# Optimization experiments

Measured on AMD Instinct MI355X. Metric: run time of the kernel, lower is better.

Reference implementation:

```python
import jax, jax.numpy as jnp
import numpy as np

N = 50000   # nodes
E = 800000  # edges (before self loops)
D = 128     # feature dim (n_feat == all n_units due to fusion-cat constraint)
BN_EPS = 1e-5


def _gcn_norm(edge_index, edge_weight, n):
    # PyG gcn_norm with add_self_loops=True (self-loop weight 1.0)
    loop = jnp.arange(n)
    row = jnp.concatenate([edge_index[0], loop])
    col = jnp.concatenate([edge_index[1], loop])
    w = jnp.concatenate([edge_weight, jnp.ones((n,), edge_weight.dtype)])
    deg = jax.ops.segment_sum(w, col, num_segments=n)  # [N]
    deg_safe = jnp.where(deg > 0, deg, 1.0)
    dis = jnp.where(deg > 0, jax.lax.rsqrt(deg_safe), 0.0)
    norm = dis[row] * w * dis[col]  # [E+N]
    return row, col, norm


def _gcn_conv(x, row, col, norm, W, b):
    # out_i = sum_{j->i} norm_ij * (x_j @ W) + b
    h = x @ W                                   # [N, Dout]
    msg = norm[:, None] * h[row]                # gather + scale, [E+N, Dout]
    out = jax.ops.segment_sum(msg, col, num_segments=x.shape[0])
    return out + b


def setup_inputs() -> dict:
    key = jax.random.key(0)
    ks = jax.random.split(key, 9)
    emb = jax.random.normal(ks[0], (N, D), jnp.float32)
    edge_index = jax.random.randint(ks[1], (2, E), 0, N)
    edge_weight = jax.random.uniform(ks[2], (E,), jnp.float32)
    W0 = jax.random.normal(ks[3], (D, D), jnp.float32) / np.sqrt(D).astype(np.float32)
    b0 = jnp.zeros((D,), jnp.float32)
    W1 = jax.random.normal(ks[4], (D, D), jnp.float32) / np.sqrt(D).astype(np.float32)
    b1 = jnp.zeros((D,), jnp.float32)
    bn_gamma = jax.random.uniform(ks[5], (D,), jnp.float32, 0.5, 1.5)
    bn_beta = jax.random.normal(ks[6], (D,), jnp.float32) * 0.1
    bn_mean = jax.random.normal(ks[7], (D,), jnp.float32) * 0.1
    bn_var = jax.random.uniform(ks[8], (D,), jnp.float32, 0.5, 1.5)
    return dict(emb=emb, edge_index=edge_index, edge_weight=edge_weight,
                W0=W0, b0=b0, W1=W1, b1=b1,
                bn_gamma=bn_gamma, bn_beta=bn_beta, bn_mean=bn_mean, bn_var=bn_var)


def reference(emb, edge_index, edge_weight, W0, b0, W1, b1,
              bn_gamma, bn_beta, bn_mean, bn_var):
    n = emb.shape[0]
    row, col, norm = _gcn_norm(edge_index, edge_weight, n)
    # loop runs once (batchnorm_stack has len 1 -> zip truncates):
    h1 = _gcn_conv(emb, row, col, norm, W0, b0)
    h1 = (h1 - bn_mean) * jax.lax.rsqrt(bn_var + BN_EPS) * bn_gamma + bn_beta
    h1 = jax.nn.elu(h1)  # dropout is identity in eval mode
    # final layer applied outside loop, no BN/ELU:
    h2 = _gcn_conv(h1, row, col, norm, W1, b1)
    # fusion: mean over [emb, h1, h2] along the stacked scale axis
    return (emb + h1 + h2) / 3.0
```

## Files before the change

### kernel.cpp

```cpp
#include <hip/hip_runtime.h>
#include <hip/hip_fp16.h>
#include <math.h>

#define BN_EPS 1e-5f
#define CAP 48
#define ABLK 8192

typedef __attribute__((ext_vector_type(8))) short bf16x8;
typedef __attribute__((ext_vector_type(4))) float f32x4;

__device__ __forceinline__ unsigned short f2b(float f) {
    unsigned u = __float_as_uint(f);
    return (unsigned short)((u + 0x7fffu + ((u >> 16) & 1u)) >> 16);
}
__device__ __forceinline__ unsigned pack2(float lo, float hi) {
    return (unsigned)f2b(lo) | ((unsigned)f2b(hi) << 16);
}
__device__ __forceinline__ float slot_w(unsigned s) {
    return __half2float(__ushort_as_half((unsigned short)(s & 0xffffu)));
}
__device__ __forceinline__ float4 b2f4(ushort4 u) {
    return make_float4(__uint_as_float((unsigned)u.x << 16),
                       __uint_as_float((unsigned)u.y << 16),
                       __uint_as_float((unsigned)u.z << 16),
                       __uint_as_float((unsigned)u.w << 16));
}

__global__ __launch_bounds__(1024) void k_bin(
        const int* __restrict__ erow, const int* __restrict__ ecol,
        const float* __restrict__ ew,
        uint2* __restrict__ binned, unsigned short* __restrict__ Hs,
        int E, int NA, int nbins,
        const float* __restrict__ W0, const float* __restrict__ W1,
        const float* __restrict__ emb,
        unsigned short* __restrict__ wp0, unsigned short* __restrict__ wp1,
        unsigned short* __restrict__ embB, int n) {
    int bb = blockIdx.x;
    int t = threadIdx.x;
    if (bb < NA) {
        __shared__ unsigned sHist[256];
        __shared__ unsigned sStart[257];
        __shared__ unsigned sCur[256];
        if (t < 256) sHist[t] = 0;
        __syncthreads();
        int base = bb * ABLK;
        int m = E - base; if (m > ABLK) m = ABLK;
        int er[8]; int ec[8]; float ewt[8];
        int i0 = t * 8;
        if (i0 + 8 <= m) {
            int4 ra = *(const int4*)(erow + base + i0);
            int4 rb = *(const int4*)(erow + base + i0 + 4);
            int4 ca = *(const int4*)(ecol + base + i0);
            int4 cb = *(const int4*)(ecol + base + i0 + 4);
            float4 wa = *(const float4*)(ew + base + i0);
            float4 wb = *(const float4*)(ew + base + i0 + 4);
            er[0] = ra.x; er[1] = ra.y; er[2] = ra.z; er[3] = ra.w;
            er[4] = rb.x; er[5] = rb.y; er[6] = rb.z; er[7] = rb.w;
            ec[0] = ca.x; ec[1] = ca.y; ec[2] = ca.z; ec[3] = ca.w;
            ec[4] = cb.x; ec[5] = cb.y; ec[6] = cb.z; ec[7] = cb.w;
            ewt[0] = wa.x; ewt[1] = wa.y; ewt[2] = wa.z; ewt[3] = wa.w;
            ewt[4] = wb.x; ewt[5] = wb.y; ewt[6] = wb.z; ewt[7] = wb.w;
        } else {
            #pragma unroll
            for (int k = 0; k < 8; ++k) {
                int i = i0 + k;
                if (i < m) { er[k] = erow[base + i]; ec[k] = ecol[base + i]; ewt[k] = ew[base + i]; }
                else { er[k] = 0; ec[k] = -1; ewt[k] = 0.f; }
            }
        }
        #pragma unroll
        for (int k = 0; k < 8; ++k)
            if (ec[k] >= 0) atomicAdd(&sHist[ec[k] >> 8], 1u);
        __syncthreads();
        if (t < 64) {
            unsigned carry = 0;
            #pragma unroll
            for (int c = 0; c < 4; ++c) {
                unsigned v = sHist[c * 64 + t];
                unsigned inc = v;
                #pragma unroll
                for (int d = 1; d < 64; d <<= 1) {
                    unsigned y = __shfl_up(inc, d);
                    if (t >= d) inc += y;
                }
                unsigned ex = carry + inc - v;
                sStart[c * 64 + t] = ex;
                sCur[c * 64 + t] = ex;
                carry += __shfl(inc, 63);
            }
            if (t == 0) sStart[256] = carry;
        }
        __syncthreads();
        if (t <= nbins) Hs[(size_t)bb * 256 + t] = (unsigned short)sStart[t];
        #pragma unroll
        for (int k = 0; k < 8; ++k) {
            if (ec[k] >= 0) {
                int bn = ec[k] >> 8;
                unsigned pos = atomicAdd(&sCur[bn], 1u);
                binned[(size_t)base + pos] =
                    make_uint2(((unsigned)er[k] << 8) | ((unsigned)ec[k] & 255u),
                               __float_as_uint(ewt[k]));
            }
        }
    } else {
        int b2 = bb - NA;
        if (b2 < 4) {
            int tid = b2 * 1024 + t;
            const float* W = (tid < 2048) ? W0 : W1;
            unsigned short* wp = (tid < 2048) ? wp0 : wp1;
            int f = tid & 2047;
            int q = f >> 9;
            int tt = (f >> 6) & 7;
            int l = f & 63;
            int col = tt * 16 + (l & 15);
            int k0 = q * 32 + (l >> 4) * 8;
            unsigned short o[8];
            #pragma unroll
            for (int j = 0; j < 8; ++j) o[j] = f2b(W[(k0 + j) * 128 + col]);
            *(uint4*)(wp + (size_t)f * 8) = *(uint4*)o;
        } else {
            int idx = (b2 - 4) * 1024 + t;
            if (idx < n * 16) {
                const float4* src = (const float4*)emb + (size_t)idx * 2;
                float4 v0 = src[0], v1 = src[1];
                uint4 o;
                o.x = pack2(v0.x, v0.y); o.y = pack2(v0.z, v0.w);
                o.z = pack2(v1.x, v1.y); o.w = pack2(v1.z, v1.w);
                ((uint4*)embB)[idx] = o;
            }
        }
    }
}

__global__ __launch_bounds__(1024) void k_build(
        const uint2* __restrict__ binned, const unsigned short* __restrict__ Hs,
        int NA, unsigned* __restrict__ eEdge, int* __restrict__ cnt,
        float* __restrict__ dis, int n) {
    __shared__ unsigned cntL[256];
    __shared__ float wsumL[256];
    int t = threadIdx.x;
    if (t < 256) { cntL[t] = 0; wsumL[t] = 0.f; }
    __syncthreads();
    int b = blockIdx.x;
    int node0 = b << 8;
    int wv = t >> 6, lane = t & 63;
    for (int s = wv; s < NA; s += 16) {
        int start = Hs[(size_t)s * 256 + b];
        int end   = Hs[(size_t)s * 256 + b + 1];
        size_t sb = (size_t)s * ABLK;
        for (int o = start + lane; o < end; o += 64) {
            uint2 rec = binned[sb + o];
            unsigned d = rec.x & 255u;
            unsigned r = rec.x >> 8;
            float w = __uint_as_float(rec.y);
            unsigned p = atomicAdd(&cntL[d], 1u);
            if (p < CAP)
                eEdge[(size_t)(node0 + (int)d) * CAP + p] =
                    (r << 16) | (unsigned)__half_as_ushort(__float2half(w));
            atomicAdd(&wsumL[d], w);
        }
    }
    __syncthreads();
    if (t < 256) {
        int node = node0 + t;
        if (node < n) {
            unsigned c = cntL[t]; if (c > CAP) c = CAP;
            cnt[node] = (int)c;
            dis[node] = rsqrtf(wsumL[t] + 1.0f);
        }
    }
}

__device__ __forceinline__ void agg_node(const unsigned* __restrict__ ep,
                                         const unsigned short* __restrict__ h,
                                         const float* __restrict__ dis,
                                         float disc, int c, int lane,
                                         float acc[8]) {
    int g = lane >> 4;
    int fo = (lane & 15) * 8;
    for (int j = 0; j < c; j += 16) {
        unsigned s[4];
        int r[4];
        float d[4], nm[4];
        uint4 u[4];
        #pragma unroll
        for (int k = 0; k < 4; ++k) s[k] = ep[j + 4 * k + g];
        #pragma unroll
        for (int k = 0; k < 4; ++k) r[k] = (j + 4 * k + g < c) ? (int)(s[k] >> 16) : 0;
        #pragma unroll
        for (int k = 0; k < 4; ++k) d[k] = dis[r[k]];
        #pragma unroll
        for (int k = 0; k < 4; ++k) u[k] = *(const uint4*)(h + ((size_t)r[k] << 7) + fo);
        #pragma unroll
        for (int k = 0; k < 4; ++k)
            nm[k] = (j + 4 * k + g < c) ? d[k] * slot_w(s[k]) * disc : 0.f;
        #pragma unroll
        for (int k = 0; k < 4; ++k) {
            acc[0] += nm[k] * __uint_as_float(u[k].x << 16);
            acc[1] += nm[k] * __uint_as_float(u[k].x & 0xffff0000u);
            acc[2] += nm[k] * __uint_as_float(u[k].y << 16);
            acc[3] += nm[k] * __uint_as_float(u[k].y & 0xffff0000u);
            acc[4] += nm[k] * __uint_as_float(u[k].z << 16);
            acc[5] += nm[k] * __uint_as_float(u[k].z & 0xffff0000u);
            acc[6] += nm[k] * __uint_as_float(u[k].w << 16);
            acc[7] += nm[k] * __uint_as_float(u[k].w & 0xffff0000u);
        }
    }
    #pragma unroll
    for (int f = 0; f < 8; ++f) {
        acc[f] += __shfl_xor(acc[f], 16);
        acc[f] += __shfl_xor(acc[f], 32);
    }
}

__global__ __launch_bounds__(1024) void k_conv1(
        const int* __restrict__ cnt, const unsigned* __restrict__ eEdge,
        const unsigned short* __restrict__ embB, const float* __restrict__ dis,
        const unsigned short* __restrict__ wp,
        const float* __restrict__ b0, const float* __restrict__ gamma,
        const float* __restrict__ beta, const float* __restrict__ mean,
        const float* __restrict__ var,
        unsigned short* __restrict__ h1b, int n) {
    __shared__ unsigned short sWp[16384];
    __shared__ unsigned short sA[16 * 136];
    int t = threadIdx.x;
    { uint4* d = (uint4*)sWp; const uint4* s = (const uint4*)wp;
      d[t] = s[t]; d[t + 1024] = s[t + 1024]; }
    int w = t >> 6;
    int lane = t & 63;
    int wid = blockIdx.x * 16 + w;
    bool valid = wid < n;
    int c = valid ? __builtin_amdgcn_readfirstlane(cnt[wid]) : 0;
    float disc = valid ? dis[wid] : 0.f;
    float acc[8] = {};
    agg_node(eEdge + (size_t)wid * CAP, embB, dis, disc, c, lane, acc);
    if (lane < 16) {
        int fo = lane * 8;
        float s2 = disc * disc;
        uint4 hu = make_uint4(0, 0, 0, 0);
        if (valid) hu = *(const uint4*)(embB + ((size_t)wid << 7) + fo);
        acc[0] += s2 * __uint_as_float(hu.x << 16);
        acc[1] += s2 * __uint_as_float(hu.x & 0xffff0000u);
        acc[2] += s2 * __uint_as_float(hu.y << 16);
        acc[3] += s2 * __uint_as_float(hu.y & 0xffff0000u);
        acc[4] += s2 * __uint_as_float(hu.z << 16);
        acc[5] += s2 * __uint_as_float(hu.z & 0xffff0000u);
        acc[6] += s2 * __uint_as_float(hu.w << 16);
        acc[7] += s2 * __uint_as_float(hu.w & 0xffff0000u);
        uint4 o;
        o.x = pack2(acc[0], acc[1]); o.y = pack2(acc[2], acc[3]);
        o.z = pack2(acc[4], acc[5]); o.w = pack2(acc[6], acc[7]);
        *(uint4*)(sA + w * 136 + fo) = o;
    }
    __syncthreads();
    int m = lane & 15, quad = lane >> 4;
    f32x4 c2 = {0.f, 0.f, 0.f, 0.f};
    if (w < 8) {
        #pragma unroll
        for (int q = 0; q < 4; ++q) {
            bf16x8 a = *(const bf16x8*)(sA + m * 136 + q * 32 + quad * 8);
            bf16x8 b = *(const bf16x8*)(sWp + (size_t)((q * 8 + w) * 64 + lane) * 8);
            c2 = __builtin_amdgcn_mfma_f32_16x16x32_bf16(a, b, c2, 0, 0, 0);
        }
    }
    __syncthreads();
    if (w < 8) {
        int col = w * 16 + m;
        float bias = b0[col];
        float mn = mean[col], bt = beta[col];
        float iv = rsqrtf(var[col] + BN_EPS) * gamma[col];
        #pragma unroll
        for (int r = 0; r < 4; ++r) {
            float x = c2[r] + bias;
            x = (x - mn) * iv + bt;
            x = x > 0.f ? x : expm1f(x);
            sA[(quad * 4 + r) * 136 + col] = f2b(x);
        }
    }
    __syncthreads();
    if (t < 256) {
        int r = t >> 4, c8 = (t & 15) * 8;
        int node = blockIdx.x * 16 + r;
        if (node < n)
            *(uint4*)(h1b + ((size_t)node << 7) + c8) = *(const uint4*)(sA + r * 136 + c8);
    }
}

__global__ __launch_bounds__(1024) void k_conv2(
        const int* __restrict__ cnt, const unsigned* __restrict__ eEdge,
        const unsigned short* __restrict__ h1b, const float* __restrict__ dis,
        const unsigned short* __restrict__ wp,
        const float* __restrict__ b1, const float* __restrict__ emb,
        float* __restrict__ out, int n) {
    __shared__ unsigned short sWp[16384];
    __shared__ unsigned short sA[16 * 136];
    __shared__ float sC[16 * 132];
    int t = threadIdx.x;
    { uint4* d = (uint4*)sWp; const uint4* s = (const uint4*)wp;
      d[t] = s[t]; d[t + 1024] = s[t + 1024]; }
    int w = t >> 6;
    int lane = t & 63;
    int wid = blockIdx.x * 16 + w;
    bool valid = wid < n;
    int c = valid ? __builtin_amdgcn_readfirstlane(cnt[wid]) : 0;
    float disc = valid ? dis[wid] : 0.f;
    float acc[8] = {};
    agg_node(eEdge + (size_t)wid * CAP, h1b, dis, disc, c, lane, acc);
    if (lane < 16) {
        int fo = lane * 8;
        float s2 = disc * disc;
        uint4 hu = make_uint4(0, 0, 0, 0);
        if (valid) hu = *(const uint4*)(h1b + ((size_t)wid << 7) + fo);
        acc[0] += s2 * __uint_as_float(hu.x << 16);
        acc[1] += s2 * __uint_as_float(hu.x & 0xffff0000u);
        acc[2] += s2 * __uint_as_float(hu.y << 16);
        acc[3] += s2 * __uint_as_float(hu.y & 0xffff0000u);
        acc[4] += s2 * __uint_as_float(hu.z << 16);
        acc[5] += s2 * __uint_as_float(hu.z & 0xffff0000u);
        acc[6] += s2 * __uint_as_float(hu.w << 16);
        acc[7] += s2 * __uint_as_float(hu.w & 0xffff0000u);
        uint4 o;
        o.x = pack2(acc[0], acc[1]); o.y = pack2(acc[2], acc[3]);
        o.z = pack2(acc[4], acc[5]); o.w = pack2(acc[6], acc[7]);
        *(uint4*)(sA + w * 136 + fo) = o;
    }
    __syncthreads();
    int m = lane & 15, quad = lane >> 4;
    f32x4 c2 = {0.f, 0.f, 0.f, 0.f};
    if (w < 8) {
        #pragma unroll
        for (int q = 0; q < 4; ++q) {
            bf16x8 a = *(const bf16x8*)(sA + m * 136 + q * 32 + quad * 8);
            bf16x8 b = *(const bf16x8*)(sWp + (size_t)((q * 8 + w) * 64 + lane) * 8);
            c2 = __builtin_amdgcn_mfma_f32_16x16x32_bf16(a, b, c2, 0, 0, 0);
        }
        int col = w * 16 + m;
        float bias = b1[col];
        #pragma unroll
        for (int r = 0; r < 4; ++r)
            sC[(quad * 4 + r) * 132 + col] = c2[r] + bias;
    }
    __syncthreads();
    if (t < 512) {
        int r = t >> 5, c4 = (t & 31) * 4;
        int node = blockIdx.x * 16 + r;
        if (node < n) {
            float4 cc = *(const float4*)(sC + r * 132 + c4);
            float4 ev = *(const float4*)(emb + ((size_t)node << 7) + c4);
            float4 hv = b2f4(*(const ushort4*)(h1b + ((size_t)node << 7) + c4));
            const float third = 1.0f / 3.0f;
            float4 o;
            o.x = (ev.x + hv.x + cc.x) * third;
            o.y = (ev.y + hv.y + cc.y) * third;
            o.z = (ev.z + hv.z + cc.z) * third;
            o.w = (ev.w + hv.w + cc.w) * third;
            *(float4*)(out + ((size_t)node << 7) + c4) = o;
        }
    }
}

extern "C" void kernel_launch(void* const* d_in, const int* in_sizes, int n_in,
                              void* d_out, int out_size, void* d_ws, size_t ws_size,
                              hipStream_t stream) {
    const float* emb   = (const float*)d_in[0];
    const int*   eidx  = (const int*)d_in[1];
    const float* ew    = (const float*)d_in[2];
    const float* W0    = (const float*)d_in[3];
    const float* b0    = (const float*)d_in[4];
    const float* W1    = (const float*)d_in[5];
    const float* b1    = (const float*)d_in[6];
    const float* gamma = (const float*)d_in[7];
    const float* beta  = (const float*)d_in[8];
    const float* mean  = (const float*)d_in[9];
    const float* var   = (const float*)d_in[10];

    const int n = in_sizes[0] / 128;
    const int E = in_sizes[2];
    const int* rowp = eidx;
    const int* colp = eidx + E;

    char* ws = (char*)d_ws;
    unsigned short* embB = (unsigned short*)ws;
    unsigned short* h1b  = (unsigned short*)(ws + (size_t)n * 256);
    uint2* binned = (uint2*)h1b;
    char* p = ws + (size_t)n * 512;
    float* dis  = (float*)p;
    int*   cnt  = (int*)  (p + (size_t)n * 4);
    unsigned short* wp0 = (unsigned short*)(p + (size_t)n * 8);
    unsigned short* wp1 = (unsigned short*)(p + (size_t)n * 8 + 32768);
    unsigned short* Hs  = (unsigned short*)(p + (size_t)n * 8 + 65536);
    unsigned* eEdge = (unsigned*)(p + (size_t)n * 8 + 131072);
    float* outf = (float*)d_out;

    const int NA    = (E + ABLK - 1) / ABLK;
    const int PB    = 4 + (n * 16 + 1023) / 1024;
    const int nbins = (n + 255) >> 8;
    const int cb    = (n + 15) / 16;

    k_bin<<<NA + PB, 1024, 0, stream>>>(rowp, colp, ew, binned, Hs, E, NA, nbins,
                                        W0, W1, emb, wp0, wp1, embB, n);
    k_build<<<nbins, 1024, 0, stream>>>(binned, Hs, NA, eEdge, cnt, dis, n);
    k_conv1<<<cb, 1024, 0, stream>>>(cnt, eEdge, embB, dis, wp0,
                                     b0, gamma, beta, mean, var, h1b, n);
    k_conv2<<<cb, 1024, 0, stream>>>(cnt, eEdge, h1b, dis, wp1,
                                     b1, emb, outf, n);
}
```

Measured before the change: 199.7 us.

## Fuse all stages into one cooperative persistent kernel with grid syncs

Merges binning, CSR build, and both GCN conv layers into a single persistent kernel launched cooperatively, separated by grid-wide syncs, with a phased multi-launch fallback. It aims to remove inter-kernel launch gaps and tail effects. Binned edge records are also staged in shared memory and written to global memory in a coalesced pass instead of scattered writes. The cost is grid-sync overhead, a grid limited by occupancy of large-shared-memory 1024-thread blocks, and fewer concurrent blocks for the build phase.

Result: slower. 652.4 us (+226.6%).

```diff
diff --git a/kernel.cpp b/kernel.cpp
--- a/kernel.cpp
+++ b/kernel.cpp
@@ -1,6 +1,9 @@
 #include <hip/hip_runtime.h>
+#include <hip/hip_cooperative_groups.h>
 #include <hip/hip_fp16.h>
 #include <math.h>
+
+namespace cg = cooperative_groups;
 
 #define BN_EPS 1e-5f
 #define CAP 48
@@ -24,151 +27,6 @@
                        __uint_as_float((unsigned)u.y << 16),
                        __uint_as_float((unsigned)u.z << 16),
                        __uint_as_float((unsigned)u.w << 16));
-}
-
-__global__ __launch_bounds__(1024) void k_bin(
-        const int* __restrict__ erow, const int* __restrict__ ecol,
-        const float* __restrict__ ew,
-        uint2* __restrict__ binned, unsigned short* __restrict__ Hs,
-        int E, int NA, int nbins,
-        const float* __restrict__ W0, const float* __restrict__ W1,
-        const float* __restrict__ emb,
-        unsigned short* __restrict__ wp0, unsigned short* __restrict__ wp1,
-        unsigned short* __restrict__ embB, int n) {
-    int bb = blockIdx.x;
-    int t = threadIdx.x;
-    if (bb < NA) {
-        __shared__ unsigned sHist[256];
-        __shared__ unsigned sStart[257];
-        __shared__ unsigned sCur[256];
-        if (t < 256) sHist[t] = 0;
-        __syncthreads();
-        int base = bb * ABLK;
-        int m = E - base; if (m > ABLK) m = ABLK;
-        int er[8]; int ec[8]; float ewt[8];
-        int i0 = t * 8;
-        if (i0 + 8 <= m) {
-            int4 ra = *(const int4*)(erow + base + i0);
-            int4 rb = *(const int4*)(erow + base + i0 + 4);
-            int4 ca = *(const int4*)(ecol + base + i0);
-            int4 cb = *(const int4*)(ecol + base + i0 + 4);
-            float4 wa = *(const float4*)(ew + base + i0);
-            float4 wb = *(const float4*)(ew + base + i0 + 4);
-            er[0] = ra.x; er[1] = ra.y; er[2] = ra.z; er[3] = ra.w;
-            er[4] = rb.x; er[5] = rb.y; er[6] = rb.z; er[7] = rb.w;
-            ec[0] = ca.x; ec[1] = ca.y; ec[2] = ca.z; ec[3] = ca.w;
-            ec[4] = cb.x; ec[5] = cb.y; ec[6] = cb.z; ec[7] = cb.w;
-            ewt[0] = wa.x; ewt[1] = wa.y; ewt[2] = wa.z; ewt[3] = wa.w;
-            ewt[4] = wb.x; ewt[5] = wb.y; ewt[6] = wb.z; ewt[7] = wb.w;
-        } else {
-            #pragma unroll
-            for (int k = 0; k < 8; ++k) {
-                int i = i0 + k;
-                if (i < m) { er[k] = erow[base + i]; ec[k] = ecol[base + i]; ewt[k] = ew[base + i]; }
-                else { er[k] = 0; ec[k] = -1; ewt[k] = 0.f; }
-            }
-        }
-        #pragma unroll
-        for (int k = 0; k < 8; ++k)
-            if (ec[k] >= 0) atomicAdd(&sHist[ec[k] >> 8], 1u);
-        __syncthreads();
-        if (t < 64) {
-            unsigned carry = 0;
-            #pragma unroll
-            for (int c = 0; c < 4; ++c) {
-                unsigned v = sHist[c * 64 + t];
-                unsigned inc = v;
-                #pragma unroll
-                for (int d = 1; d < 64; d <<= 1) {
-                    unsigned y = __shfl_up(inc, d);
-                    if (t >= d) inc += y;
-                }
-                unsigned ex = carry + inc - v;
-                sStart[c * 64 + t] = ex;
-                sCur[c * 64 + t] = ex;
-                carry += __shfl(inc, 63);
-            }
-            if (t == 0) sStart[256] = carry;
-        }
-        __syncthreads();
-        if (t <= nbins) Hs[(size_t)bb * 256 + t] = (unsigned short)sStart[t];
-        #pragma unroll
-        for (int k = 0; k < 8; ++k) {
-            if (ec[k] >= 0) {
-                int bn = ec[k] >> 8;
-                unsigned pos = atomicAdd(&sCur[bn], 1u);
-                binned[(size_t)base + pos] =
-                    make_uint2(((unsigned)er[k] << 8) | ((unsigned)ec[k] & 255u),
-                               __float_as_uint(ewt[k]));
-            }
-        }
-    } else {
-        int b2 = bb - NA;
-        if (b2 < 4) {
-            int tid = b2 * 1024 + t;
-            const float* W = (tid < 2048) ? W0 : W1;
-            unsigned short* wp = (tid < 2048) ? wp0 : wp1;
-            int f = tid & 2047;
-            int q = f >> 9;
-            int tt = (f >> 6) & 7;
-            int l = f & 63;
-            int col = tt * 16 + (l & 15);
-            int k0 = q * 32 + (l >> 4) * 8;
-            unsigned short o[8];
-            #pragma unroll
-            for (int j = 0; j < 8; ++j) o[j] = f2b(W[(k0 + j) * 128 + col]);
-            *(uint4*)(wp + (size_t)f * 8) = *(uint4*)o;
-        } else {
-            int idx = (b2 - 4) * 1024 + t;
-            if (idx < n * 16) {
-                const float4* src = (const float4*)emb + (size_t)idx * 2;
-                float4 v0 = src[0], v1 = src[1];
-                uint4 o;
-                o.x = pack2(v0.x, v0.y); o.y = pack2(v0.z, v0.w);
-                o.z = pack2(v1.x, v1.y); o.w = pack2(v1.z, v1.w);
-                ((uint4*)embB)[idx] = o;
-            }
-        }
-    }
-}
-
-__global__ __launch_bounds__(1024) void k_build(
-        const uint2* __restrict__ binned, const unsigned short* __restrict__ Hs,
-        int NA, unsigned* __restrict__ eEdge, int* __restrict__ cnt,
-        float* __restrict__ dis, int n) {
-    __shared__ unsigned cntL[256];
-    __shared__ float wsumL[256];
-    int t = threadIdx.x;
-    if (t < 256) { cntL[t] = 0; wsumL[t] = 0.f; }
-    __syncthreads();
-    int b = blockIdx.x;
-    int node0 = b << 8;
-    int wv = t >> 6, lane = t & 63;
-    for (int s = wv; s < NA; s += 16) {
-        int start = Hs[(size_t)s * 256 + b];
-        int end   = Hs[(size_t)s * 256 + b + 1];
-        size_t sb = (size_t)s * ABLK;
-        for (int o = start + lane; o < end; o += 64) {
-            uint2 rec = binned[sb + o];
-            unsigned d = rec.x & 255u;
-            unsigned r = rec.x >> 8;
-            float w = __uint_as_float(rec.y);
-            unsigned p = atomicAdd(&cntL[d], 1u);
-            if (p < CAP)
-                eEdge[(size_t)(node0 + (int)d) * CAP + p] =
-                    (r << 16) | (unsigned)__half_as_ushort(__float2half(w));
-            atomicAdd(&wsumL[d], w);
-        }
-    }
-    __syncthreads();
-    if (t < 256) {
-        int node = node0 + t;
-        if (node < n) {
-            unsigned c = cntL[t]; if (c > CAP) c = CAP;
-            cnt[node] = (int)c;
-            dis[node] = rsqrtf(wsumL[t] + 1.0f);
-        }
-    }
 }
 
 __device__ __forceinline__ void agg_node(const unsigned* __restrict__ ep,
@@ -213,148 +71,301 @@
     }
 }
 
-__global__ __launch_bounds__(1024) void k_conv1(
-        const int* __restrict__ cnt, const unsigned* __restrict__ eEdge,
-        const unsigned short* __restrict__ embB, const float* __restrict__ dis,
-        const unsigned short* __restrict__ wp,
-        const float* __restrict__ b0, const float* __restrict__ gamma,
-        const float* __restrict__ beta, const float* __restrict__ mean,
-        const float* __restrict__ var,
-        unsigned short* __restrict__ h1b, int n) {
-    __shared__ unsigned short sWp[16384];
-    __shared__ unsigned short sA[16 * 136];
+__global__ __launch_bounds__(1024, 8) void k_mega(
+        const int* __restrict__ erow, const int* __restrict__ ecol,
+        const float* __restrict__ ew,
+        uint2* __restrict__ binned, unsigned short* __restrict__ Hs,
+        unsigned* __restrict__ eEdge, int* __restrict__ cnt, float* __restrict__ dis,
+        const float* __restrict__ W0, const float* __restrict__ W1,
+        const float* __restrict__ emb,
+        unsigned short* __restrict__ wp0, unsigned short* __restrict__ wp1,
+        unsigned short* __restrict__ embB,
+        const float* __restrict__ b0v, const float* __restrict__ gammav,
+        const float* __restrict__ betav, const float* __restrict__ meanv,
+        const float* __restrict__ varv, const float* __restrict__ b1v,
+        unsigned short* __restrict__ h1b, float* __restrict__ out,
+        int n, int E, int NA, int PB, int phase) {
+    __shared__ __align__(16) char smem[68624];
     int t = threadIdx.x;
-    { uint4* d = (uint4*)sWp; const uint4* s = (const uint4*)wp;
-      d[t] = s[t]; d[t + 1024] = s[t + 1024]; }
+    const int nblk = gridDim.x;
+    const int gb = (n + 255) >> 8;
+    const int cb = (n + 15) >> 4;
+
+    if (phase == 0 || phase == 1) {
+        unsigned* sHist  = (unsigned*)smem;
+        unsigned* sStart = sHist + 256;
+        unsigned* sCur   = sStart + 257;
+        uint2*    sRec   = (uint2*)(smem + 3080);
+        for (int item = blockIdx.x; item < NA + PB; item += nblk) {
+            __syncthreads();
+            if (item < NA) {
+                if (t < 256) sHist[t] = 0;
+                __syncthreads();
+                int base = item * ABLK;
+                int m = E - base; if (m > ABLK) m = ABLK;
+                int er[8]; int ec[8]; float ewt[8];
+                int i0 = t * 8;
+                if (i0 + 8 <= m) {
+                    int4 ra = *(const int4*)(erow + base + i0);
+                    int4 rb = *(const int4*)(erow + base + i0 + 4);
+                    int4 ca = *(const int4*)(ecol + base + i0);
+                    int4 cb4 = *(const int4*)(ecol + base + i0 + 4);
+                    float4 wa = *(const float4*)(ew + base + i0);
+                    float4 wb = *(const float4*)(ew + base + i0 + 4);
+                    er[0] = ra.x; er[1] = ra.y; er[2] = ra.z; er[3] = ra.w;
+                    er[4] = rb.x; er[5] = rb.y; er[6] = rb.z; er[7] = rb.w;
+                    ec[0] = ca.x; ec[1] = ca.y; ec[2] = ca.z; ec[3] = ca.w;
+                    ec[4] = cb4.x; ec[5] = cb4.y; ec[6] = cb4.z; ec[7] = cb4.w;
+                    ewt[0] = wa.x; ewt[1] = wa.y; ewt[2] = wa.z; ewt[3] = wa.w;
+                    ewt[4] = wb.x; ewt[5] = wb.y; ewt[6] = wb.z; ewt[7] = wb.w;
+                } else {
+                    #pragma unroll
+                    for (int k = 0; k < 8; ++k) {
+                        int i = i0 + k;
+                        if (i < m) { er[k] = erow[base + i]; ec[k] = ecol[base + i]; ewt[k] = ew[base + i]; }
+                        else { er[k] = 0; ec[k] = -1; ewt[k] = 0.f; }
+                    }
+                }
+                #pragma unroll
+                for (int k = 0; k < 8; ++k)
+                    if (ec[k] >= 0) atomicAdd(&sHist[ec[k] >> 8], 1u);
+                __syncthreads();
+                if (t < 64) {
+                    unsigned carry = 0;
+                    #pragma unroll
+                    for (int c4 = 0; c4 < 4; ++c4) {
+                        unsigned v = sHist[c4 * 64 + t];
+                        unsigned inc = v;
+                        #pragma unroll
+                        for (int d = 1; d < 64; d <<= 1) {
+                            unsigned y = __shfl_up(inc, d);
+                            if (t >= d) inc += y;
+                        }
+                        unsigned ex = carry + inc - v;
+                        sStart[c4 * 64 + t] = ex;
+                        sCur[c4 * 64 + t] = ex;
+                        carry += __shfl(inc, 63);
+                    }
+                    if (t == 0) sStart[256] = carry;
+                }
+                __syncthreads();
+                if (t <= gb) Hs[(size_t)item * 256 + t] = (unsigned short)sStart[t];
+                #pragma unroll
+                for (int k = 0; k < 8; ++k) {
+                    if (ec[k] >= 0) {
+                        int bn = ec[k] >> 8;
+                        unsigned pos = atomicAdd(&sCur[bn], 1u);
+                        sRec[pos] = make_uint2(((unsigned)er[k] << 8) | ((unsigned)ec[k] & 255u),
+                                               __float_as_uint(ewt[k]));
+                    }
+                }
+                __syncthreads();
+                for (int i = t; i < m; i += 1024) binned[(size_t)base + i] = sRec[i];
+            } else {
+                int b2 = item - NA;
+                if (b2 < 4) {
+                    int tid = b2 * 1024 + t;
+                    const float* W = (tid < 2048) ? W0 : W1;
+                    unsigned short* wp = (tid < 2048) ? wp0 : wp1;
+                    int f = tid & 2047;
+                    int q = f >> 9;
+                    int tt = (f >> 6) & 7;
+                    int l = f & 63;
+                    int col = tt * 16 + (l & 15);
+                    int k0 = q * 32 + (l >> 4) * 8;
+                    unsigned short o[8];
+                    #pragma unroll
+                    for (int j = 0; j < 8; ++j) o[j] = f2b(W[(k0 + j) * 128 + col]);
+                    *(uint4*)(wp + (size_t)f * 8) = *(uint4*)o;
+                } else {
+                    int idx = (b2 - 4) * 1024 + t;
+                    if (idx < n * 16) {
+                        const float4* src = (const float4*)emb + (size_t)idx * 2;
+                        float4 v0 = src[0], v1 = src[1];
+                        uint4 o;
+                        o.x = pack2(v0.x, v0.y); o.y = pack2(v0.z, v0.w);
+                        o.z = pack2(v1.x, v1.y); o.w = pack2(v1.z, v1.w);
+                        ((uint4*)embB)[idx] = o;
+                    }
+                }
+            }
+        }
+    }
+    if (phase == 0) { __threadfence(); cg::this_grid().sync(); }
+
+    if (phase == 0 || phase == 2) {
+        unsigned* cntL = (unsigned*)smem;
+        float* wsumL = (float*)(smem + 1024);
+        for (int b = blockIdx.x; b < gb; b += nblk) {
+            __syncthreads();
+            if (t < 256) { cntL[t] = 0; wsumL[t] = 0.f; }
+            __syncthreads();
+            int node0 = b << 8;
+            int wv = t >> 6, lane = t & 63;
+            for (int s = wv; s < NA; s += 16) {
+                int start = Hs[(size_t)s * 256 + b];
+                int end   = Hs[(size_t)s * 256 + b + 1];
+                size_t sb = (size_t)s * ABLK;
+                for (int o = start + lane; o < end; o += 64) {
+                    uint2 rec = binned[sb + o];
+                    unsigned d = rec.x & 255u;
+                    unsigned r = rec.x >> 8;
+                    float w = __uint_as_float(rec.y);
+                    unsigned p = atomicAdd(&cntL[d], 1u);
+                    if (p < CAP)
+                        eEdge[(size_t)(node0 + (int)d) * CAP + p] =
+                            (r << 16) | (unsigned)__half_as_ushort(__float2half(w));
+                    atomicAdd(&wsumL[d], w);
+                }
+            }
+            __syncthreads();
+            if (t < 256) {
+                int node = node0 + t;
+                if (node < n) {
+                    unsigned c = cntL[t]; if (c > CAP) c = CAP;
+                    cnt[node] = (int)c;
+                    dis[node] = rsqrtf(wsumL[t] + 1.0f);
+                }
+            }
+        }
+    }
+    if (phase == 0) { __threadfence(); cg::this_grid().sync(); }
+
     int w = t >> 6;
     int lane = t & 63;
-    int wid = blockIdx.x * 16 + w;
-    bool valid = wid < n;
-    int c = valid ? __builtin_amdgcn_readfirstlane(cnt[wid]) : 0;
-    float disc = valid ? dis[wid] : 0.f;
-    float acc[8] = {};
-    agg_node(eEdge + (size_t)wid * CAP, embB, dis, disc, c, lane, acc);
-    if (lane < 16) {
-        int fo = lane * 8;
-        float s2 = disc * disc;
-        uint4 hu = make_uint4(0, 0, 0, 0);
-        if (valid) hu = *(const uint4*)(embB + ((size_t)wid << 7) + fo);
-        acc[0] += s2 * __uint_as_float(hu.x << 16);
-        acc[1] += s2 * __uint_as_float(hu.x & 0xffff0000u);
-        acc[2] += s2 * __uint_as_float(hu.y << 16);
-        acc[3] += s2 * __uint_as_float(hu.y & 0xffff0000u);
-        acc[4] += s2 * __uint_as_float(hu.z << 16);
-        acc[5] += s2 * __uint_as_float(hu.z & 0xffff0000u);
-        acc[6] += s2 * __uint_as_float(hu.w << 16);
-        acc[7] += s2 * __uint_as_float(hu.w & 0xffff0000u);
-        uint4 o;
-        o.x = pack2(acc[0], acc[1]); o.y = pack2(acc[2], acc[3]);
-        o.z = pack2(acc[4], acc[5]); o.w = pack2(acc[6], acc[7]);
-        *(uint4*)(sA + w * 136 + fo) = o;
-    }
-    __syncthreads();
-    int m = lane & 15, quad = lane >> 4;
-    f32x4 c2 = {0.f, 0.f, 0.f, 0.f};
-    if (w < 8) {
-        #pragma unroll
-        for (int q = 0; q < 4; ++q) {
-            bf16x8 a = *(const bf16x8*)(sA + m * 136 + q * 32 + quad * 8);
-            bf16x8 b = *(const bf16x8*)(sWp + (size_t)((q * 8 + w) * 64 + lane) * 8);
-            c2 = __builtin_amdgcn_mfma_f32_16x16x32_bf16(a, b, c2, 0, 0, 0);
+    unsigned short* sWp = (unsigned short*)smem;
+    unsigned short* sA  = (unsigned short*)(smem + 32768);
+    float* sC           = (float*)(smem + 37120);
+
+    if (phase == 0 || phase == 3) {
+        { uint4* d = (uint4*)sWp; const uint4* s = (const uint4*)wp0;
+          d[t] = s[t]; d[t + 1024] = s[t + 1024]; }
+        __syncthreads();
+        for (int bin = blockIdx.x; bin < cb; bin += nblk) {
+            int wid = bin * 16 + w;
+            bool valid = wid < n;
+            int c = valid ? __builtin_amdgcn_readfirstlane(cnt[wid]) : 0;
+            float disc = valid ? dis[wid] : 0.f;
+            float acc[8] = {};
+            agg_node(eEdge + (size_t)wid * CAP, embB, dis, disc, c, lane, acc);
+            if (lane < 16) {
+                int fo = lane * 8;
+                float s2 = disc * disc;
+                uint4 hu = make_uint4(0, 0, 0, 0);
+                if (valid) hu = *(const uint4*)(embB + ((size_t)wid << 7) + fo);
+                acc[0] += s2 * __uint_as_float(hu.x << 16);
+                acc[1] += s2 * __uint_as_float(hu.x & 0xffff0000u);
+                acc[2] += s2 * __uint_as_float(hu.y << 16);
+                acc[3] += s2 * __uint_as_float(hu.y & 0xffff0000u);
+                acc[4] += s2 * __uint_as_float(hu.z << 16);
+                acc[5] += s2 * __uint_as_float(hu.z & 0xffff0000u);
+                acc[6] += s2 * __uint_as_float(hu.w << 16);
+                acc[7] += s2 * __uint_as_float(hu.w & 0xffff0000u);
+                uint4 o;
+                o.x = pack2(acc[0], acc[1]); o.y = pack2(acc[2], acc[3]);
+                o.z = pack2(acc[4], acc[5]); o.w = pack2(acc[6], acc[7]);
+                *(uint4*)(sA + w * 136 + fo) = o;
+            }
+            __syncthreads();
+            int mm = lane & 15, quad = lane >> 4;
+            f32x4 c2 = {0.f, 0.f, 0.f, 0.f};
+            if (w < 8) {
+                #pragma unroll
+                for (int q = 0; q < 4; ++q) {
+                    bf16x8 a = *(const bf16x8*)(sA + mm * 136 + q * 32 + quad * 8);
+                    bf16x8 b = *(const bf16x8*)(sWp + (size_t)((q * 8 + w) * 64 + lane) * 8);
+                    c2 = __builtin_amdgcn_mfma_f32_16x16x32_bf16(a, b, c2, 0, 0, 0);
+                }
+            }
+            __syncthreads();
+            if (w < 8) {
+                int col = w * 16 + mm;
+                float bias = b0v[col];
+                float mn = meanv[col], bt = betav[col];
+                float iv = rsqrtf(varv[col] + BN_EPS) * gammav[col];
+                #pragma unroll
+                for (int r = 0; r < 4; ++r) {
+                    float x = c2[r] + bias;
+                    x = (x - mn) * iv + bt;
+                    x = x > 0.f ? x : expm1f(x);
+                    sA[(quad * 4 + r) * 136 + col] = f2b(x);
+                }
+            }
+            __syncthreads();
+            if (t < 256) {
+                int r = t >> 4, c8 = (t & 15) * 8;
+                int node = bin * 16 + r;
+                if (node < n)
+                    *(uint4*)(h1b + ((size_t)node << 7) + c8) = *(const uint4*)(sA + r * 136 + c8);
+            }
+            __syncthreads();
         }
     }
-    __syncthreads();
-    if (w < 8) {
-        int col = w * 16 + m;
-        float bias = b0[col];
-        float mn = mean[col], bt = beta[col];
-        float iv = rsqrtf(var[col] + BN_EPS) * gamma[col];
-        #pragma unroll
-        for (int r = 0; r < 4; ++r) {
-            float x = c2[r] + bias;
-            x = (x - mn) * iv + bt;
-            x = x > 0.f ? x : expm1f(x);
-            sA[(quad * 4 + r) * 136 + col] = f2b(x);
-        }
-    }
-    __syncthreads();
-    if (t < 256) {
-        int r = t >> 4, c8 = (t & 15) * 8;
-        int node = blockIdx.x * 16 + r;
-        if (node < n)
-            *(uint4*)(h1b + ((size_t)node << 7) + c8) = *(const uint4*)(sA + r * 136 + c8);
-    }
-}
-
-__global__ __launch_bounds__(1024) void k_conv2(
-        const int* __restrict__ cnt, const unsigned* __restrict__ eEdge,
-        const unsigned short* __restrict__ h1b, const float* __restrict__ dis,
-        const unsigned short* __restrict__ wp,
-        const float* __restrict__ b1, const float* __restrict__ emb,
-        float* __restrict__ out, int n) {
-    __shared__ unsigned short sWp[16384];
-    __shared__ unsigned short sA[16 * 136];
-    __shared__ float sC[16 * 132];
-    int t = threadIdx.x;
-    { uint4* d = (uint4*)sWp; const uint4* s = (const uint4*)wp;
-      d[t] = s[t]; d[t + 1024] = s[t + 1024]; }
-    int w = t >> 6;
-    int lane = t & 63;
-    int wid = blockIdx.x * 16 + w;
-    bool valid = wid < n;
-    int c = valid ? __builtin_amdgcn_readfirstlane(cnt[wid]) : 0;
-    float disc = valid ? dis[wid] : 0.f;
-    float acc[8] = {};
-    agg_node(eEdge + (size_t)wid * CAP, h1b, dis, disc, c, lane, acc);
-    if (lane < 16) {
-        int fo = lane * 8;
-        float s2 = disc * disc;
-        uint4 hu = make_uint4(0, 0, 0, 0);
-        if (valid) hu = *(const uint4*)(h1b + ((size_t)wid << 7) + fo);
-        acc[0] += s2 * __uint_as_float(hu.x << 16);
-        acc[1] += s2 * __uint_as_float(hu.x & 0xffff0000u);
-        acc[2] += s2 * __uint_as_float(hu.y << 16);
-        acc[3] += s2 * __uint_as_float(hu.y & 0xffff0000u);
-        acc[4] += s2 * __uint_as_float(hu.z << 16);
-        acc[5] += s2 * __uint_as_float(hu.z & 0xffff0000u);
-        acc[6] += s2 * __uint_as_float(hu.w << 16);
-        acc[7] += s2 * __uint_as_float(hu.w & 0xffff0000u);
-        uint4 o;
-        o.x = pack2(acc[0], acc[1]); o.y = pack2(acc[2], acc[3]);
-        o.z = pack2(acc[4], acc[5]); o.w = pack2(acc[6], acc[7]);
-        *(uint4*)(sA + w * 136 + fo) = o;
-    }
-    __syncthreads();
-    int m = lane & 15, quad = lane >> 4;
-    f32x4 c2 = {0.f, 0.f, 0.f, 0.f};
-    if (w < 8) {
-        #pragma unroll
-        for (int q = 0; q < 4; ++q) {
-            bf16x8 a = *(const bf16x8*)(sA + m * 136 + q * 32 + quad * 8);
-            bf16x8 b = *(const bf16x8*)(sWp + (size_t)((q * 8 + w) * 64 + lane) * 8);
-            c2 = __builtin_amdgcn_mfma_f32_16x16x32_bf16(a, b, c2, 0, 0, 0);
-        }
-        int col = w * 16 + m;
-        float bias = b1[col];
-        #pragma unroll
-        for (int r = 0; r < 4; ++r)
-            sC[(quad * 4 + r) * 132 + col] = c2[r] + bias;
-    }
-    __syncthreads();
-    if (t < 512) {
-        int r = t >> 5, c4 = (t & 31) * 4;
-        int node = blockIdx.x * 16 + r;
-        if (node < n) {
-            float4 cc = *(const float4*)(sC + r * 132 + c4);
-            float4 ev = *(const float4*)(emb + ((size_t)node << 7) + c4);
-            float4 hv = b2f4(*(const ushort4*)(h1b + ((size_t)node << 7) + c4));
-            const float third = 1.0f / 3.0f;
-            float4 o;
-            o.x = (ev.x + hv.x + cc.x) * third;
-            o.y = (ev.y + hv.y + cc.y) * third;
-            o.z = (ev.z + hv.z + cc.z) * third;
-            o.w = (ev.w + hv.w + cc.w) * third;
-            *(float4*)(out + ((size_t)node << 7) + c4) = o;
+    if (phase == 0) { __threadfence(); cg::this_grid().sync(); }
+
+    if (phase == 0 || phase == 4) {
+        { uint4* d = (uint4*)sWp; const uint4* s = (const uint4*)wp1;
+          d[t] = s[t]; d[t + 1024] = s[t + 1024]; }
+        __syncthreads();
+        for (int bin = blockIdx.x; bin < cb; bin += nblk) {
+            int wid = bin * 16 + w;
+            bool valid = wid < n;
+            int c = valid ? __builtin_amdgcn_readfirstlane(cnt[wid]) : 0;
+            float disc = valid ? dis[wid] : 0.f;
+            float acc[8] = {};
+            agg_node(eEdge + (size_t)wid * CAP, h1b, dis, disc, c, lane, acc);
+            if (lane < 16) {
+                int fo = lane * 8;
+                float s2 = disc * disc;
+                uint4 hu = make_uint4(0, 0, 0, 0);
+                if (valid) hu = *(const uint4*)(h1b + ((size_t)wid << 7) + fo);
+                acc[0] += s2 * __uint_as_float(hu.x << 16);
+                acc[1] += s2 * __uint_as_float(hu.x & 0xffff0000u);
+                acc[2] += s2 * __uint_as_float(hu.y << 16);
+                acc[3] += s2 * __uint_as_float(hu.y & 0xffff0000u);
+                acc[4] += s2 * __uint_as_float(hu.z << 16);
+                acc[5] += s2 * __uint_as_float(hu.z & 0xffff0000u);
+                acc[6] += s2 * __uint_as_float(hu.w << 16);
+                acc[7] += s2 * __uint_as_float(hu.w & 0xffff0000u);
+                uint4 o;
+                o.x = pack2(acc[0], acc[1]); o.y = pack2(acc[2], acc[3]);
+                o.z = pack2(acc[4], acc[5]); o.w = pack2(acc[6], acc[7]);
+                *(uint4*)(sA + w * 136 + fo) = o;
+            }
+            __syncthreads();
+            int mm = lane & 15, quad = lane >> 4;
+            f32x4 c2 = {0.f, 0.f, 0.f, 0.f};
+            if (w < 8) {
+                #pragma unroll
+                for (int q = 0; q < 4; ++q) {
+                    bf16x8 a = *(const bf16x8*)(sA + mm * 136 + q * 32 + quad * 8);
+                    bf16x8 b = *(const bf16x8*)(sWp + (size_t)((q * 8 + w) * 64 + lane) * 8);
+                    c2 = __builtin_amdgcn_mfma_f32_16x16x32_bf16(a, b, c2, 0, 0, 0);
+                }
+                int col = w * 16 + mm;
+                float bias = b1v[col];
+                #pragma unroll
+                for (int r = 0; r < 4; ++r)
+                    sC[(quad * 4 + r) * 132 + col] = c2[r] + bias;
+            }
+            __syncthreads();
+            if (t < 512) {
+                int r = t >> 5, c4 = (t & 31) * 4;
+                int node = bin * 16 + r;
+                if (node < n) {
+                    float4 cc = *(const float4*)(sC + r * 132 + c4);
+                    float4 ev = *(const float4*)(emb + ((size_t)node << 7) + c4);
+                    float4 hv = b2f4(*(const ushort4*)(h1b + ((size_t)node << 7) + c4));
+                    const float third = 1.0f / 3.0f;
+                    float4 o;
+                    o.x = (ev.x + hv.x + cc.x) * third;
+                    o.y = (ev.y + hv.y + cc.y) * third;
+                    o.z = (ev.z + hv.z + cc.z) * third;
+                    o.w = (ev.w + hv.w + cc.w) * third;
+                    *(float4*)(out + ((size_t)node << 7) + c4) = o;
+                }
+            }
+            __syncthreads();
         }
     }
 }
@@ -379,29 +390,68 @@
     const int* rowp = eidx;
     const int* colp = eidx + E;
 
+    const int NA = (E + ABLK - 1) / ABLK;
+    const int PB = 4 + (n * 16 + 1023) / 1024;
+    const int gb = (n + 255) / 256;
+    const int cb = (n + 15) / 16;
+
     char* ws = (char*)d_ws;
     unsigned short* embB = (unsigned short*)ws;
     unsigned short* h1b  = (unsigned short*)(ws + (size_t)n * 256);
     uint2* binned = (uint2*)h1b;
     char* p = ws + (size_t)n * 512;
-    float* dis  = (float*)p;
-    int*   cnt  = (int*)  (p + (size_t)n * 4);
+    float* dis = (float*)p;
+    int*   cnt = (int*)(p + (size_t)n * 4);
     unsigned short* wp0 = (unsigned short*)(p + (size_t)n * 8);
     unsigned short* wp1 = (unsigned short*)(p + (size_t)n * 8 + 32768);
     unsigned short* Hs  = (unsigned short*)(p + (size_t)n * 8 + 65536);
     unsigned* eEdge = (unsigned*)(p + (size_t)n * 8 + 131072);
     float* outf = (float*)d_out;
 
-    const int NA    = (E + ABLK - 1) / ABLK;
-    const int PB    = 4 + (n * 16 + 1023) / 1024;
-    const int nbins = (n + 255) >> 8;
-    const int cb    = (n + 15) / 16;
-
-    k_bin<<<NA + PB, 1024, 0, stream>>>(rowp, colp, ew, binned, Hs, E, NA, nbins,
-                                        W0, W1, emb, wp0, wp1, embB, n);
-    k_build<<<nbins, 1024, 0, stream>>>(binned, Hs, NA, eEdge, cnt, dis, n);
-    k_conv1<<<cb, 1024, 0, stream>>>(cnt, eEdge, embB, dis, wp0,
-                                     b0, gamma, beta, mean, var, h1b, n);
-    k_conv2<<<cb, 1024, 0, stream>>>(cnt, eEdge, h1b, dis, wp1,
-                                     b1, emb, outf, n);
-}
+    static int s_grid = -1, s_coop = 0;
+    if (s_grid < 0) {
+        int perCU = 0, cus = 0, coop = 0, dev = 0;
+        hipGetDevice(&dev);
+        hipOccupancyMaxActiveBlocksPerMultiprocessor(&perCU, k_mega, 1024, 0);
+        hipDeviceGetAttribute(&cus, hipDeviceAttributeMultiprocessorCount, dev);
+        hipDeviceGetAttribute(&coop, hipDeviceAttributeCooperativeLaunch, dev);
+        if (perCU < 1) { perCU = 1; coop = 0; }
+        if (cus < 1) cus = 256;
+        s_grid = perCU * cus;
+        s_coop = coop;
+    }
+
+    if (s_coop) {
+        int phase = 0;
+        int nn = n, EE = E, NAv = NA, PBv = PB;
+        void* args[] = {
+            (void*)&rowp, (void*)&colp, (void*)&ew,
+            (void*)&binned, (void*)&Hs,
+            (void*)&eEdge, (void*)&cnt, (void*)&dis,
+            (void*)&W0, (void*)&W1, (void*)&emb,
+            (void*)&wp0, (void*)&wp1, (void*)&embB,
+            (void*)&b0, (void*)&gamma, (void*)&beta, (void*)&mean, (void*)&var,
+            (void*)&b1, (void*)&h1b, (void*)&outf,
+            (void*)&nn, (void*)&EE, (void*)&NAv, (void*)&PBv, (void*)&phase
+        };
+        hipLaunchCooperativeKernel((const void*)k_mega, dim3(s_grid), dim3(1024),
+                                   args, 0, stream);
+    } else {
+        k_mega<<<NA + PB, 1024, 0, stream>>>(rowp, colp, ew, binned, Hs, eEdge, cnt, dis,
+                                             W0, W1, emb, wp0, wp1, embB,
+                                             b0, gamma, beta, mean, var, b1, h1b, outf,
+                                             n, E, NA, PB, 1);
+        k_mega<<<gb, 1024, 0, stream>>>(rowp, colp, ew, binned, Hs, eEdge, cnt, dis,
+                                        W0, W1, emb, wp0, wp1, embB,
+                                        b0, gamma, beta, mean, var, b1, h1b, outf,
+                                        n, E, NA, PB, 2);
+        k_mega<<<cb, 1024, 0, stream>>>(rowp, colp, ew, binned, Hs, eEdge, cnt, dis,
+                                        W0, W1, emb, wp0, wp1, embB,
+                                        b0, gamma, beta, mean, var, b1, h1b, outf,
+                                        n, E, NA, PB, 3);
+        k_mega<<<cb, 1024, 0, stream>>>(rowp, colp, ew, binned, Hs, eEdge, cnt, dis,
+                                        W0, W1, emb, wp0, wp1, embB,
+                                        b0, gamma, beta, mean, var, b1, h1b, outf,
+                                        n, E, NA, PB, 4);
+    }
+}
```
